# Kernel tuning notes

Hardware: AMD Instinct MI355X
Metric: run time of the kernel (lower is better)

## Reference

```python
import jax, jax.numpy as jnp
import numpy as np

PRED_STEPS = 5
NEG = 16
C = 256
B = 64
H = 16
W = 16
SKIP = 1
EPS = 1e-11


def setup_inputs() -> dict:
    key = jax.random.key(0)
    ks = jax.random.split(key, 3 + PRED_STEPS)
    inp = {
        "z": jax.random.normal(ks[0], (B, C, H, W), jnp.float32),
        "c": jax.random.normal(ks[1], (B, C, H, W), jnp.float32),
        "Wk": jax.random.normal(ks[2], (PRED_STEPS, C, C), jnp.float32) * 0.05,
    }
    for k in range(1, PRED_STEPS + 1):
        rows = (H - k - SKIP) * W * B
        inp[f"rand_idx_{k}"] = jax.random.randint(ks[2 + k], (rows * NEG,), 0, rows, dtype=jnp.int64 if jax.config.jax_enable_x64 else jnp.int32)
    return inp


def reference(z, c, Wk, rand_idx_1, rand_idx_2, rand_idx_3, rand_idx_4, rand_idx_5):
    idx_list = [rand_idx_1, rand_idx_2, rand_idx_3, rand_idx_4, rand_idx_5]
    total_loss = jnp.float32(0.0)
    patchwise_loss = jnp.zeros((B, H, W), jnp.float32)
    patchwise_count = jnp.zeros((H, W), jnp.float32)
    for k in range(1, PRED_STEPS + 1):
        off = k + SKIP
        Hk = H - off
        # 1x1 conv projection, permuted to [Hk, W, B, C]
        ztwk = jnp.einsum('oi,bihw->hwbo', Wk[k - 1], z[:, :, off:, :])
        # random-gather negatives: [Hk, W, B, NEG, C]
        flat = ztwk.reshape(Hk * W * B, C)
        ztwk_shuf = flat[idx_list[k - 1]].reshape(Hk, W, B, NEG, C)
        # context: [Hk, W, B, C]
        ctx = jnp.transpose(c[:, :, :Hk, :], (2, 3, 0, 1))
        # scoring
        main = jnp.einsum('hwbc,hwbc->hwb', ctx, ztwk)[..., None]        # [Hk,W,B,1]
        negs = jnp.einsum('hwbc,hwbnc->hwbn', ctx, ztwk_shuf)            # [Hk,W,B,NEG]
        logits = jnp.concatenate([main, negs], axis=-1)                  # [Hk,W,B,1+NEG]
        log_fk = jnp.transpose(logits, (2, 3, 0, 1))                     # [B,1+NEG,Hk,W]
        sm = jax.nn.softmax(log_fk, axis=1)
        stu_loss = -jnp.log(sm[:, 0, :, :] + EPS)                        # [B,Hk,W]
        total_loss = total_loss + stu_loss.mean()
        patchwise_loss = patchwise_loss.at[:, off:, :].add(stu_loss)
        patchwise_loss = patchwise_loss.at[:, :H - off, :].add(stu_loss)
        ones = jnp.ones((Hk, W), jnp.float32)
        patchwise_count = patchwise_count.at[off:, :].add(ones)
        patchwise_count = patchwise_count.at[:H - off, :].add(ones)
    total_loss = total_loss / PRED_STEPS
    return (total_loss, patchwise_loss, patchwise_count)
```

## Files before the change

### kernel.cpp

```cpp
#include <hip/hip_runtime.h>
#include <hip/hip_bf16.h>
#include <math.h>

#define NEG_ 16
#define PRED_ 5
#define EPS_ 1e-11f
#define LDW 18
#define GSTR 272
#define ASTR 72

typedef __attribute__((ext_vector_type(8))) short bf16x8;
typedef __attribute__((ext_vector_type(4))) float f32x4;

static __device__ __forceinline__ unsigned short f2bu(float f) {
  __hip_bfloat16 h = __float2bfloat16(f);
  return *(unsigned short*)&h;
}


__global__ __launch_bounds__(256) void prep_all(
    const float* __restrict__ z, const float* __restrict__ c,
    const float* __restrict__ Wk,
    unsigned short* __restrict__ Zp, unsigned short* __restrict__ Cb,
    unsigned short* __restrict__ Wb, float* __restrict__ out) {
  __shared__ float tile[32][65];
  const int t = threadIdx.x;
  if (blockIdx.x == 0 && blockIdx.y == 0 && blockIdx.z == 0 && t == 0)
    out[0] = 0.f;
  if (blockIdx.y == 7) {
    int ib = blockIdx.z * 256 + blockIdx.x;
    if (ib < 320) {
      const int k = ib >> 6, tl = ib & 63;
      const int r0 = (tl >> 3) * 32, c0g = (tl & 7) * 32;
      const int tx = t & 31, ty = t >> 5;
#pragma unroll
      for (int r = 0; r < 32; r += 8)
        tile[ty + r][tx] = Wk[k * 65536 + (r0 + ty + r) * 256 + c0g + tx];
      __syncthreads();
#pragma unroll
      for (int r = 0; r < 32; r += 8)
        Wb[k * 65536 + (c0g + ty + r) * 256 + r0 + tx] = f2bu(tile[tx][ty + r]);
    }
    return;
  }
  const float* in = blockIdx.z ? c : z;
  unsigned short* out2 = blockIdx.z ? Cb : Zp;
  const int p0 = blockIdx.x * 64;
  const int q0 = blockIdx.y * 32 + (blockIdx.z ? 0 : 32);
  const int tx = t & 31, ty = t >> 5;
#pragma unroll
  for (int r = 0; r < 64; r += 8)
    tile[tx][ty + r] = in[(size_t)(p0 + ty + r) * 256 + q0 + tx];
  __syncthreads();
  const int pp = t & 63, wq = t >> 6;
#pragma unroll
  for (int r = 0; r < 32; r += 4)
    out2[(size_t)(q0 + wq + r) * 16384 + p0 + pp] = f2bu(tile[wq + r][pp]);
}

__global__ __launch_bounds__(256) void gemm_all(
    const unsigned short* __restrict__ Cb, const unsigned short* __restrict__ Wb,
    unsigned short* __restrict__ Cw) {
  const int kk = blockIdx.z;
  const int Mk = (14 - kk) * 1024;
  const int m0b = blockIdx.y * 128;
  if (m0b >= Mk) return;
  const unsigned short* A = Cb;
  const unsigned short* Wm = Wb + (size_t)kk * 65536;
  unsigned short* Y = Cw + (size_t)kk * 14336 * 256;
  __shared__ unsigned short As[128 * ASTR];
  __shared__ unsigned short Bs[128 * ASTR];
  const int t = threadIdx.x;
  const int wid = t >> 6, lane = t & 63;
  const int wm = wid >> 1, wn = wid & 1;
  const int l15 = lane & 15, quad = lane >> 4;
  const int n0 = blockIdx.x * 128;
  const int srow = t >> 1, shalf = t & 1;
  const unsigned short* ga = A + (size_t)(m0b + srow) * 256 + shalf * 32;
  const unsigned short* gb = Wm + (size_t)(n0 + srow) * 256 + shalf * 32;
  unsigned short* wa = As + srow * ASTR + shalf * 32;
  unsigned short* wb = Bs + srow * ASTR + shalf * 32;
  f32x4 acc[4][4] = {};
  bf16x8 ra[4], rb[4];
#pragma unroll
  for (int cs = 0; cs < 4; ++cs) {
    ra[cs] = *(const bf16x8*)(ga + cs * 8);
    rb[cs] = *(const bf16x8*)(gb + cs * 8);
  }
#pragma unroll
  for (int ki = 0; ki < 4; ++ki) {
    __syncthreads();
#pragma unroll
    for (int cs = 0; cs < 4; ++cs) {
      *(bf16x8*)(wa + cs * 8) = ra[cs];
      *(bf16x8*)(wb + cs * 8) = rb[cs];
    }
    __syncthreads();
    if (ki < 3) {
      const int k1 = (ki + 1) * 64;
#pragma unroll
      for (int cs = 0; cs < 4; ++cs) {
        ra[cs] = *(const bf16x8*)(ga + k1 + cs * 8);
        rb[cs] = *(const bf16x8*)(gb + k1 + cs * 8);
      }
    }
#pragma unroll
    for (int ks = 0; ks < 2; ++ks) {
      bf16x8 af[4], bf[4];
#pragma unroll
      for (int tm = 0; tm < 4; ++tm)
        af[tm] = *(const bf16x8*)(As + (wm * 64 + tm * 16 + l15) * ASTR + ks * 32 + quad * 8);
#pragma unroll
      for (int tn = 0; tn < 4; ++tn)
        bf[tn] = *(const bf16x8*)(Bs + (wn * 64 + tn * 16 + l15) * ASTR + ks * 32 + quad * 8);
#pragma unroll
      for (int tm = 0; tm < 4; ++tm)
#pragma unroll
        for (int tn = 0; tn < 4; ++tn)
          acc[tm][tn] = __builtin_amdgcn_mfma_f32_16x16x32_bf16(
              af[tm], bf[tn], acc[tm][tn], 0, 0, 0);
    }
  }
#pragma unroll
  for (int tm = 0; tm < 4; ++tm)
#pragma unroll
    for (int tn = 0; tn < 4; ++tn)
#pragma unroll
      for (int r = 0; r < 4; ++r)
        Y[(size_t)(m0b + wm * 64 + tm * 16 + quad * 4 + r) * 256 +
          n0 + wn * 64 + tn * 16 + l15] = f2bu(acc[tm][tn][r]);
}

__global__ __launch_bounds__(256) void score_all(
    const unsigned short* __restrict__ Cw, const unsigned short* __restrict__ Zp,
    const int* __restrict__ r1, const int* __restrict__ r2,
    const int* __restrict__ r3, const int* __restrict__ r4,
    const int* __restrict__ r5, float* __restrict__ Lk) {
  __shared__ __align__(16) unsigned short gbuf[4][16 * GSTR];
  __shared__ float L[16 * LDW];
  const int wv = threadIdx.x >> 6, lane = threadIdx.x & 63;
  const int gid = blockIdx.x;
  int kk, base;
  if (gid < 896)       { kk = 0; base = 0; }
  else if (gid < 1728) { kk = 1; base = 896; }
  else if (gid < 2496) { kk = 2; base = 1728; }
  else if (gid < 3200) { kk = 3; base = 2496; }
  else                 { kk = 4; base = 3200; }
  const int Mk = (14 - kk) * 1024;
  const int m0 = (gid - base) * 16;
  const int* ridx = kk == 0 ? r1 : kk == 1 ? r2 : kk == 2 ? r3 : kk == 3 ? r4 : r5;
  const unsigned short* Yc = Cw + (size_t)kk * 14336 * 256;
  const unsigned short* Z  = Zp + (size_t)(kk + 2) * 1024 * 256;
  const int l15 = lane & 15, quad = lane >> 4;
  const int half = lane >> 5, ch = lane & 31;
  unsigned short* mybuf = gbuf[wv];

  auto gather = [&](const unsigned short* src, int ivv, bf16x8* dst) {
#pragma unroll
    for (int j = 0; j < 8; ++j) {
      int rlo = __shfl(ivv, 2 * j);
      int rhi = __shfl(ivv, 2 * j + 1);
      int row = half ? rhi : rlo;
      dst[j] = *(const bf16x8*)(src + (size_t)row * 256 + ch * 8);
    }
  };
  auto stage = [&](const bf16x8* g) {
#pragma unroll
    for (int j2 = 0; j2 < 8; ++j2)
      *(bf16x8*)(mybuf + (2 * j2 + half) * GSTR + ch * 8) = g[j2];
  };

  const int c0 = (wv == 0) ? 0 : (wv == 1) ? 4 : (wv == 2) ? 9 : 13;
  const int nc = (wv == 1) ? 5 : 4;
  int iv[5];
#pragma unroll
  for (int j = 0; j < 5; ++j) {
    if (j < nc) {
      const int c = c0 + j;
      if (c == 0) iv[j] = m0 + l15;
      else {
        int idx = ridx[(m0 + (c - 1)) * NEG_ + l15];
        iv[j] = idx < 0 ? 0 : (idx >= Mk ? Mk - 1 : idx);
      }
    } else iv[j] = 0;
  }

  bf16x8 g[8], gn[8];
  gather(Z, iv[0], g);

  if (wv == 0) {
    bf16x8 y[8];
    gather(Yc, m0 + l15, y);
    stage(y);
  }
  __syncthreads();
  bf16x8 af[8];
#pragma unroll
  for (int tv = 0; tv < 8; ++tv)
    af[tv] = *(const bf16x8*)(gbuf[0] + l15 * GSTR + quad * 8 + tv * 32);
  __syncthreads();

  for (int j = 0; j < nc; ++j) {
    if (j + 1 < nc) gather(Z, iv[j + 1], gn);
    stage(g);
    f32x4 acc = {};
#pragma unroll
    for (int tv = 0; tv < 8; ++tv) {
      bf16x8 bfv = *(const bf16x8*)(mybuf + l15 * GSTR + quad * 8 + tv * 32);
      acc = __builtin_amdgcn_mfma_f32_16x16x32_bf16(af[tv], bfv, acc, 0, 0, 0);
    }
    const int c = c0 + j;
    if (c == 0) {
#pragma unroll
      for (int r = 0; r < 4; ++r)
        if (l15 == quad * 4 + r) L[(quad * 4 + r) * LDW] = acc[r];
    } else {
      const int i = c - 1;
      if (quad == (i >> 2)) L[i * LDW + 1 + l15] = acc[i & 3];
    }
#pragma unroll
    for (int tv = 0; tv < 8; ++tv) g[tv] = gn[tv];
  }
  __syncthreads();
  if (threadIdx.x < 16) {
    float mainv = L[threadIdx.x * LDW];
    float mx = mainv;
    float nv[NEG_];
#pragma unroll
    for (int n = 0; n < NEG_; ++n) {
      nv[n] = L[threadIdx.x * LDW + 1 + n];
      mx = fmaxf(mx, nv[n]);
    }
    float num = __expf(mainv - mx);
    float se = num;
#pragma unroll
    for (int n = 0; n < NEG_; ++n) se += __expf(nv[n] - mx);
    Lk[kk * 14336 + m0 + threadIdx.x] = -logf(num / se + EPS_);
  }
}

__global__ __launch_bounds__(256) void finalize_pl(
    const float* __restrict__ Lk, float* __restrict__ out) {
  if (blockIdx.x < 64) {
    int idx = blockIdx.x * 256 + threadIdx.x;
    int b = idx >> 8, h = (idx >> 4) & 15, w = idx & 15;
    float v = 0.f;
#pragma unroll
    for (int kk = 0; kk < PRED_; ++kk) {
      int off = kk + 2;
      if (h >= off)      v += Lk[kk * 14336 + ((h - off) * 16 + w) * 64 + b];
      if (h <= 15 - off) v += Lk[kk * 14336 + (h * 16 + w) * 64 + b];
    }
    out[1 + idx] = v;
    if (idx < 256) {
      int hh = idx >> 4;
      float cnt = 0.f;
#pragma unroll
      for (int off = 2; off <= 6; ++off)
        cnt += (hh >= off ? 1.f : 0.f) + (hh <= 15 - off ? 1.f : 0.f);
      out[1 + 16384 + idx] = cnt;
    }
  } else {
    __shared__ float red[4];
    const int cb = blockIdx.x - 64;
    const int kk = cb < 14 ? 0 : cb < 27 ? 1 : cb < 39 ? 2 : cb < 50 ? 3 : 4;
    const int s0 = kk == 0 ? 0 : kk == 1 ? 14 : kk == 2 ? 27 : kk == 3 ? 39 : 50;
    const float scale = 1.0f / (5120.0f * (float)(14 - kk));
    const int e = (cb - s0) * 1024 + threadIdx.x * 4;
    float4 v = *(const float4*)&Lk[kk * 14336 + e];
    float local = (v.x + v.y + v.z + v.w) * scale;
#pragma unroll
    for (int s = 32; s; s >>= 1) local += __shfl_down(local, s);
    if ((threadIdx.x & 63) == 0) red[threadIdx.x >> 6] = local;
    __syncthreads();
    if (threadIdx.x == 0)
      atomicAdd(out, red[0] + red[1] + red[2] + red[3]);
  }
}

extern "C" void kernel_launch(void* const* d_in, const int* in_sizes, int n_in,
                              void* d_out, int out_size, void* d_ws, size_t ws_size,
                              hipStream_t stream) {
  const float* z  = (const float*)d_in[0];
  const float* c  = (const float*)d_in[1];
  const float* Wk = (const float*)d_in[2];
  float* out = (float*)d_out;
  char* wsb = (char*)d_ws;
  unsigned short* Zp = (unsigned short*)(wsb);
  unsigned short* Cb = (unsigned short*)(wsb + 8388608);
  unsigned short* Wb = (unsigned short*)(wsb + 16777216);
  unsigned short* Cw = (unsigned short*)(wsb + 17432576);
  float*          Lk = (float*)(wsb + 54132736);

  prep_all<<<dim3(256, 8, 2), 256, 0, stream>>>(z, c, Wk, Zp, Cb, Wb, out);
  gemm_all<<<dim3(2, 112, PRED_), 256, 0, stream>>>(Cb, Wb, Cw);
  score_all<<<3840, 256, 0, stream>>>(
      Cw, Zp, (const int*)d_in[3], (const int*)d_in[4], (const int*)d_in[5],
      (const int*)d_in[6], (const int*)d_in[7], Lk);
  finalize_pl<<<124, 256, 0, stream>>>(Lk, out);
}
```

Measured before the change: 154.2 us.

## Gather negatives from an fp8 copy of z and score with split-fp8 MFMA

The prep kernel now also writes an fp8 copy of z. The score kernel gathers the 16 random negative rows from that 1-byte copy instead of the bf16 copy, which halves the gather bytes. The context row is split into high and low fp8 parts so two fp8 MFMAs keep some extra precision. The main positive score still uses bf16, and the work is rebalanced so wave 0 does the positive plus one negative and the other waves do five negatives each. The risk is that fp8 rounding of the negatives changes the logits enough to fail tolerance, and the extra fp8 write adds traffic to prep.

```diff
diff --git a/kernel.cpp b/kernel.cpp
--- a/kernel.cpp
+++ b/kernel.cpp
@@ -7,10 +7,12 @@
 #define EPS_ 1e-11f
 #define LDW 18
 #define GSTR 272
+#define R8 272
 #define ASTR 72
 
 typedef __attribute__((ext_vector_type(8))) short bf16x8;
 typedef __attribute__((ext_vector_type(4))) float f32x4;
+typedef __attribute__((ext_vector_type(2))) float f32x2;
 
 static __device__ __forceinline__ unsigned short f2bu(float f) {
   __hip_bfloat16 h = __float2bfloat16(f);
@@ -22,7 +24,8 @@
     const float* __restrict__ z, const float* __restrict__ c,
     const float* __restrict__ Wk,
     unsigned short* __restrict__ Zp, unsigned short* __restrict__ Cb,
-    unsigned short* __restrict__ Wb, float* __restrict__ out) {
+    unsigned short* __restrict__ Wb, unsigned char* __restrict__ Zp8,
+    float* __restrict__ out) {
   __shared__ float tile[32][65];
   const int t = threadIdx.x;
   if (blockIdx.x == 0 && blockIdx.y == 0 && blockIdx.z == 0 && t == 0)
@@ -54,8 +57,14 @@
   __syncthreads();
   const int pp = t & 63, wq = t >> 6;
 #pragma unroll
-  for (int r = 0; r < 32; r += 4)
-    out2[(size_t)(q0 + wq + r) * 16384 + p0 + pp] = f2bu(tile[wq + r][pp]);
+  for (int r = 0; r < 32; r += 4) {
+    float v = tile[wq + r][pp];
+    out2[(size_t)(q0 + wq + r) * 16384 + p0 + pp] = f2bu(v);
+    if (!blockIdx.z) {
+      int b8 = __builtin_amdgcn_cvt_pk_fp8_f32(v, 0.f, 0, false);
+      Zp8[(size_t)(q0 + wq + r) * 16384 + p0 + pp] = (unsigned char)(b8 & 0xff);
+    }
+  }
 }
 
 __global__ __launch_bounds__(256) void gemm_all(
@@ -133,10 +142,12 @@
 
 __global__ __launch_bounds__(256) void score_all(
     const unsigned short* __restrict__ Cw, const unsigned short* __restrict__ Zp,
+    const unsigned char* __restrict__ Zp8,
     const int* __restrict__ r1, const int* __restrict__ r2,
     const int* __restrict__ r3, const int* __restrict__ r4,
     const int* __restrict__ r5, float* __restrict__ Lk) {
-  __shared__ __align__(16) unsigned short gbuf[4][16 * GSTR];
+  __shared__ __align__(16) unsigned short gbufB[16 * GSTR];
+  __shared__ __align__(16) unsigned char g8buf[4][16 * R8];
   __shared__ float L[16 * LDW];
   const int wv = threadIdx.x >> 6, lane = threadIdx.x & 63;
   const int gid = blockIdx.x;
@@ -151,11 +162,12 @@
   const int* ridx = kk == 0 ? r1 : kk == 1 ? r2 : kk == 2 ? r3 : kk == 3 ? r4 : r5;
   const unsigned short* Yc = Cw + (size_t)kk * 14336 * 256;
   const unsigned short* Z  = Zp + (size_t)(kk + 2) * 1024 * 256;
+  const unsigned char*  Z8 = Zp8 + (size_t)(kk + 2) * 1024 * 256;
   const int l15 = lane & 15, quad = lane >> 4;
   const int half = lane >> 5, ch = lane & 31;
-  unsigned short* mybuf = gbuf[wv];
-
-  auto gather = [&](const unsigned short* src, int ivv, bf16x8* dst) {
+  unsigned char* my8 = g8buf[wv];
+
+  auto gatherB = [&](const unsigned short* src, int ivv, bf16x8* dst) {
 #pragma unroll
     for (int j = 0; j < 8; ++j) {
       int rlo = __shfl(ivv, 2 * j);
@@ -164,62 +176,115 @@
       dst[j] = *(const bf16x8*)(src + (size_t)row * 256 + ch * 8);
     }
   };
-  auto stage = [&](const bf16x8* g) {
+  auto stageB = [&](const bf16x8* g) {
 #pragma unroll
     for (int j2 = 0; j2 < 8; ++j2)
-      *(bf16x8*)(mybuf + (2 * j2 + half) * GSTR + ch * 8) = g[j2];
-  };
-
-  const int c0 = (wv == 0) ? 0 : (wv == 1) ? 4 : (wv == 2) ? 9 : 13;
-  const int nc = (wv == 1) ? 5 : 4;
-  int iv[5];
+      *(bf16x8*)(gbufB + (2 * j2 + half) * GSTR + ch * 8) = g[j2];
+  };
+  auto gather8 = [&](int ivv, uint4* dst) {
+#pragma unroll
+    for (int j = 0; j < 4; ++j) {
+      int row = __shfl(ivv, 4 * j + quad);
+      dst[j] = *(const uint4*)(Z8 + (size_t)row * 256 + l15 * 16);
+    }
+  };
+  auto stage8 = [&](const uint4* h) {
+#pragma unroll
+    for (int j = 0; j < 4; ++j)
+      *(uint4*)(my8 + (4 * j + quad) * R8 + l15 * 16) = h[j];
+  };
+
+  const int i0 = (wv == 0) ? 0 : (wv - 1) * 5 + 1;
+  const int n8 = (wv == 0) ? 1 : 5;
+  int iv8[5];
 #pragma unroll
   for (int j = 0; j < 5; ++j) {
-    if (j < nc) {
-      const int c = c0 + j;
-      if (c == 0) iv[j] = m0 + l15;
-      else {
-        int idx = ridx[(m0 + (c - 1)) * NEG_ + l15];
-        iv[j] = idx < 0 ? 0 : (idx >= Mk ? Mk - 1 : idx);
-      }
-    } else iv[j] = 0;
-  }
-
-  bf16x8 g[8], gn[8];
-  gather(Z, iv[0], g);
+    if (j < n8) {
+      int idx = ridx[(m0 + (i0 + j)) * NEG_ + l15];
+      iv8[j] = idx < 0 ? 0 : (idx >= Mk ? Mk - 1 : idx);
+    } else iv8[j] = 0;
+  }
+
+  bf16x8 gm[8];
+  uint4 hA[4], hB[4];
+  if (wv == 0) {
+    gatherB(Z, m0 + l15, gm);
+    gather8(iv8[0], hA);
+  } else {
+    gather8(iv8[0], hA);
+    gather8(iv8[1], hB);
+  }
 
   if (wv == 0) {
     bf16x8 y[8];
-    gather(Yc, m0 + l15, y);
-    stage(y);
+    gatherB(Yc, m0 + l15, y);
+    stageB(y);
   }
   __syncthreads();
   bf16x8 af[8];
 #pragma unroll
   for (int tv = 0; tv < 8; ++tv)
-    af[tv] = *(const bf16x8*)(gbuf[0] + l15 * GSTR + quad * 8 + tv * 32);
+    af[tv] = *(const bf16x8*)(gbufB + l15 * GSTR + quad * 8 + tv * 32);
+  long af8h[8], af8l[8];
+#pragma unroll
+  for (int tv = 0; tv < 8; ++tv) {
+    float f[8];
+#pragma unroll
+    for (int e = 0; e < 8; ++e) {
+      union { unsigned u; float fl; } cv;
+      cv.u = ((unsigned)(unsigned short)af[tv][e]) << 16;
+      f[e] = cv.fl;
+    }
+    int lo = 0, hi = 0;
+    lo = __builtin_amdgcn_cvt_pk_fp8_f32(f[0], f[1], lo, false);
+    lo = __builtin_amdgcn_cvt_pk_fp8_f32(f[2], f[3], lo, true);
+    hi = __builtin_amdgcn_cvt_pk_fp8_f32(f[4], f[5], hi, false);
+    hi = __builtin_amdgcn_cvt_pk_fp8_f32(f[6], f[7], hi, true);
+    af8h[tv] = (long)(((unsigned long)(unsigned)hi << 32) | (unsigned)lo);
+    f32x2 d01 = __builtin_amdgcn_cvt_pk_f32_fp8(lo, false);
+    f32x2 d23 = __builtin_amdgcn_cvt_pk_f32_fp8(lo, true);
+    f32x2 d45 = __builtin_amdgcn_cvt_pk_f32_fp8(hi, false);
+    f32x2 d67 = __builtin_amdgcn_cvt_pk_f32_fp8(hi, true);
+    int lo2 = 0, hi2 = 0;
+    lo2 = __builtin_amdgcn_cvt_pk_fp8_f32(f[0] - d01[0], f[1] - d01[1], lo2, false);
+    lo2 = __builtin_amdgcn_cvt_pk_fp8_f32(f[2] - d23[0], f[3] - d23[1], lo2, true);
+    hi2 = __builtin_amdgcn_cvt_pk_fp8_f32(f[4] - d45[0], f[5] - d45[1], hi2, false);
+    hi2 = __builtin_amdgcn_cvt_pk_fp8_f32(f[6] - d67[0], f[7] - d67[1], hi2, true);
+    af8l[tv] = (long)(((unsigned long)(unsigned)hi2 << 32) | (unsigned)lo2);
+  }
   __syncthreads();
 
-  for (int j = 0; j < nc; ++j) {
-    if (j + 1 < nc) gather(Z, iv[j + 1], gn);
-    stage(g);
+  auto chain8 = [&](uint4* buf, int jp2, int i) {
+    stage8(buf);
+    if (jp2 < n8) gather8(iv8[jp2], buf);
+    f32x4 a = {};
+#pragma unroll
+    for (int tv = 0; tv < 8; ++tv) {
+      long bv = *(const long*)(my8 + l15 * R8 + tv * 32 + quad * 8);
+      a = __builtin_amdgcn_mfma_f32_16x16x32_fp8_fp8(af8h[tv], bv, a, 0, 0, 0);
+      a = __builtin_amdgcn_mfma_f32_16x16x32_fp8_fp8(af8l[tv], bv, a, 0, 0, 0);
+    }
+    if (quad == (i >> 2)) L[i * LDW + 1 + l15] = a[i & 3];
+  };
+
+  if (wv == 0) {
+    stageB(gm);
     f32x4 acc = {};
 #pragma unroll
     for (int tv = 0; tv < 8; ++tv) {
-      bf16x8 bfv = *(const bf16x8*)(mybuf + l15 * GSTR + quad * 8 + tv * 32);
+      bf16x8 bfv = *(const bf16x8*)(gbufB + l15 * GSTR + quad * 8 + tv * 32);
       acc = __builtin_amdgcn_mfma_f32_16x16x32_bf16(af[tv], bfv, acc, 0, 0, 0);
     }
-    const int c = c0 + j;
-    if (c == 0) {
-#pragma unroll
-      for (int r = 0; r < 4; ++r)
-        if (l15 == quad * 4 + r) L[(quad * 4 + r) * LDW] = acc[r];
-    } else {
-      const int i = c - 1;
-      if (quad == (i >> 2)) L[i * LDW + 1 + l15] = acc[i & 3];
-    }
-#pragma unroll
-    for (int tv = 0; tv < 8; ++tv) g[tv] = gn[tv];
+#pragma unroll
+    for (int r = 0; r < 4; ++r)
+      if (l15 == quad * 4 + r) L[(quad * 4 + r) * LDW] = acc[r];
+    chain8(hA, 99, 0);
+  } else {
+    chain8(hA, 2, i0 + 0);
+    chain8(hB, 3, i0 + 1);
+    chain8(hA, 4, i0 + 2);
+    chain8(hB, 99, i0 + 3);
+    chain8(hA, 99, i0 + 4);
   }
   __syncthreads();
   if (threadIdx.x < 16) {
@@ -286,16 +351,17 @@
   const float* Wk = (const float*)d_in[2];
   float* out = (float*)d_out;
   char* wsb = (char*)d_ws;
-  unsigned short* Zp = (unsigned short*)(wsb);
-  unsigned short* Cb = (unsigned short*)(wsb + 8388608);
-  unsigned short* Wb = (unsigned short*)(wsb + 16777216);
-  unsigned short* Cw = (unsigned short*)(wsb + 17432576);
-  float*          Lk = (float*)(wsb + 54132736);
-
-  prep_all<<<dim3(256, 8, 2), 256, 0, stream>>>(z, c, Wk, Zp, Cb, Wb, out);
+  unsigned short* Zp  = (unsigned short*)(wsb);
+  unsigned short* Cb  = (unsigned short*)(wsb + 8388608);
+  unsigned short* Wb  = (unsigned short*)(wsb + 16777216);
+  unsigned short* Cw  = (unsigned short*)(wsb + 17432576);
+  float*          Lk  = (float*)(wsb + 54132736);
+  unsigned char*  Zp8 = (unsigned char*)(wsb + 54525952);
+
+  prep_all<<<dim3(256, 8, 2), 256, 0, stream>>>(z, c, Wk, Zp, Cb, Wb, Zp8, out);
   gemm_all<<<dim3(2, 112, PRED_), 256, 0, stream>>>(Cb, Wb, Cw);
   score_all<<<3840, 256, 0, stream>>>(
-      Cw, Zp, (const int*)d_in[3], (const int*)d_in[4], (const int*)d_in[5],
+      Cw, Zp, Zp8, (const int*)d_in[3], (const int*)d_in[4], (const int*)d_in[5],
       (const int*)d_in[6], (const int*)d_in[7], Lk);
   finalize_pl<<<124, 256, 0, stream>>>(Lk, out);
 }
```

Result: slower. 201.1 us (+30.4%).
